# Kernel optimization log

Measured on AMD Instinct MI355X. Metric: run time of the kernel, lower is better.

Reference implementation:

```python
import jax, jax.numpy as jnp
import numpy as np


def setup_inputs() -> dict:
    key = jax.random.key(0)
    k1, k2, k3, k4 = jax.random.split(key, 4)
    H = W = 1024
    B = 16
    image = jax.random.normal(k1, (1, H, W), dtype=jnp.float32)
    x = jax.random.normal(k2, (B, 1, H, W), dtype=jnp.float32)
    # Conv2d(1, 9, 3) parameters, torch layout: weight (out=9, in=1, 3, 3), bias (9,)
    fan_in = 1 * 3 * 3
    bound = 1.0 / np.sqrt(fan_in)
    W_KL = jax.random.uniform(k3, (9, 1, 3, 3), jnp.float32, -bound, bound)
    b_KL = jax.random.uniform(k4, (9,), jnp.float32, -bound, bound)
    return {"image": image, "x": x, "W_KL": W_KL, "b_KL": b_KL}


def reference(image, x, W_KL, b_KL):
    # K = Conv2d(image): (1,H,W) -> (9,H,W), 'same' padding
    K = jax.lax.conv_general_dilated(
        image[None], W_KL, window_strides=(1, 1), padding='SAME',
        dimension_numbers=('NCHW', 'OIHW', 'NCHW'))[0] + b_KL[:, None, None]
    H, W = image.shape[1], image.shape[2]
    # permute (9,H,W) -> (H,W,9) -> unflatten to per-pixel 3x3 kernels (H,W,3,3)
    K = jnp.transpose(K, (1, 2, 0)).reshape(H, W, 3, 3)
    # Apply spatially-varying 3x3 kernel: y[b,c,h,w] = sum_{a,d} K[h,w,a,d] * x_pad[b,c,h+a,w+d]
    x_pad = jnp.pad(x, ((0, 0), (0, 0), (1, 1), (1, 1)))
    y = jnp.zeros_like(x)
    for a in range(3):
        for d in range(3):
            y = y + K[:, :, a, d] * x_pad[:, :, a:a + H, d:d + W]
    return y
```

## Files before the change

kernel.cpp:

```cpp
#include <hip/hip_runtime.h>

#define IH 1024
#define IW 1024
#define NB 16

typedef float v4f __attribute__((ext_vector_type(4)));

__device__ __forceinline__ void glds16(const float* g, float* l) {
    __builtin_amdgcn_global_load_lds(
        (const __attribute__((address_space(1))) void*)g,
        (__attribute__((address_space(3))) void*)l, 16, 0, 0);
}

struct RawWin { v4f mv[3]; float fl[3]; float fr[3]; };

__device__ __forceinline__ void issue_win(const float* __restrict__ plane,
                                          int h, int w0, RawWin& rw) {
#pragma unroll
    for (int a = 0; a < 3; ++a) {
        const int hh = h + a - 1;
        const int hc = (hh < 0) ? 0 : (hh >= IH ? IH - 1 : hh);
        const float* rowp = plane + (size_t)hc * IW;
        rw.fl[a] = rowp[w0 > 0 ? w0 - 1 : 0];
        rw.mv[a] = *(const v4f*)(rowp + w0);
        rw.fr[a] = rowp[w0 + 4 < IW ? w0 + 4 : IW - 1];
    }
}

__device__ __forceinline__ void fin_win_img(const RawWin& rw, int h, int w0,
                                            float win[3][6]) {
#pragma unroll
    for (int a = 0; a < 3; ++a) {
        const int hh = h + a - 1;
        const bool rowok = (hh >= 0) & (hh < IH);
        win[a][0] = (rowok && w0 > 0)      ? rw.fl[a]   : 0.f;
        win[a][1] = rowok ? rw.mv[a].x : 0.f;
        win[a][2] = rowok ? rw.mv[a].y : 0.f;
        win[a][3] = rowok ? rw.mv[a].z : 0.f;
        win[a][4] = rowok ? rw.mv[a].w : 0.f;
        win[a][5] = (rowok && w0 + 4 < IW) ? rw.fr[a]   : 0.f;
    }
}

__global__ __launch_bounds__(256, 4) void fused_dbuf(
    const float* __restrict__ image,
    const float* __restrict__ x,
    const float* __restrict__ Wk,
    const float* __restrict__ bk,
    float* __restrict__ out)
{
    __shared__ float lds[2][6][256];

    const int tx = threadIdx.x;
    const int wv = threadIdx.y;

    const int hwid  = blockIdx.x;
    const int xcd   = hwid & 7;
    const int chunk = hwid >> 3;
    const int bx    = chunk & 3;
    const int g     = xcd * 32 + (chunk >> 2);
    const int c0    = bx * 256;
    const int h0    = g * 4;
    const int h     = h0 + wv;
    const int lc    = tx * 4;
    const int w0    = c0 + lc;

    const size_t plane = (size_t)IH * IW;

    int zv; asm("v_mov_b32 %0, 0" : "=v"(zv));

    auto stage = [&](int b, int buf) {
        const float* xb = x + (size_t)b * plane;
        int gr = h0 - 1 + wv; gr = gr < 0 ? 0 : gr;
        glds16(xb + (size_t)gr * IW + c0 + tx * 4, &lds[buf][wv][0]);
        if (wv < 2) {
            int g2 = h0 + 3 + wv; g2 = g2 > IH - 1 ? IH - 1 : g2;
            glds16(xb + (size_t)g2 * IW + c0 + tx * 4, &lds[buf][wv + 4][0]);
        }
    };
    auto halo = [&](int b, float* HL, float* HR) {
        const float* xb = x + (size_t)b * plane;
        const int cl = (c0 > 0) ? c0 - 1 : 0;
        const int cr = (c0 + 256 < IW) ? c0 + 256 : IW - 1;
#pragma unroll
        for (int a = 0; a < 3; ++a) {
            int gr = h + a - 1; gr = gr < 0 ? 0 : (gr > IH - 1 ? IH - 1 : gr);
            const float* rp = xb + (size_t)gr * IW;
            HL[a] = rp[cl + zv];
            HR[a] = rp[cr + zv];
        }
    };

    RawWin rimg;
    issue_win(image, h, w0, rimg);
    stage(0, 0);
    float hl[2][3], hr[2][3];
    halo(0, hl[0], hr[0]);

    float wkk[81];
#pragma unroll
    for (int i = 0; i < 81; ++i) wkk[i] = Wk[i];
    float bb[9];
#pragma unroll
    for (int c = 0; c < 9; ++c) bb[c] = bk[c];

    float p[3][6];
    fin_win_img(rimg, h, w0, p);
    float Kv[4][9];
#pragma unroll
    for (int j = 0; j < 4; ++j)
#pragma unroll
        for (int c = 0; c < 9; ++c) {
            float acc = bb[c];
#pragma unroll
            for (int a = 0; a < 3; ++a)
#pragma unroll
                for (int d = 0; d < 3; ++d)
                    acc = fmaf(wkk[c * 9 + a * 3 + d], p[a][j + d], acc);
            Kv[j][c] = acc;
        }
    {
        const bool top = (h == 0);
        const bool bot = (h == IH - 1);
#pragma unroll
        for (int j = 0; j < 4; ++j)
#pragma unroll
            for (int d = 0; d < 3; ++d) {
                Kv[j][d]     = top ? 0.f : Kv[j][d];
                Kv[j][6 + d] = bot ? 0.f : Kv[j][6 + d];
            }
    }

    asm volatile("s_waitcnt vmcnt(6)" ::: "memory");
    __builtin_amdgcn_sched_barrier(0);
    __builtin_amdgcn_s_barrier();
    __builtin_amdgcn_sched_barrier(0);

    v4f yv[2];
    float* obp = out + (size_t)h * IW + w0;

#pragma unroll
    for (int b = 0; b < NB; ++b) {
        if (b > 0)
            __builtin_nontemporal_store(yv[(b - 1) & 1],
                                        (v4f*)(obp + (size_t)(b - 1) * plane));
        if (b + 1 < NB) {
            stage(b + 1, (b + 1) & 1);
            halo(b + 1, hl[(b + 1) & 1], hr[(b + 1) & 1]);
        }
        {
            const int ll = (tx > 0)  ? lc - 4 : 0;
            const int lr = (tx < 63) ? lc + 4 : 252;
            const float* lb = &lds[b & 1][0][0];
            float win[3][6];
#pragma unroll
            for (int a = 0; a < 3; ++a) {
                const float* rowp = lb + (wv + a) * 256;
                const v4f lv = *(const v4f*)(rowp + ll);
                const v4f mv = *(const v4f*)(rowp + lc);
                const v4f rv = *(const v4f*)(rowp + lr);
                const float le = (tx == 0)  ? hl[b & 1][a] : lv.w;
                const float re = (tx == 63) ? hr[b & 1][a] : rv.x;
                win[a][0] = (w0 > 0)      ? le : 0.f;
                win[a][1] = mv.x; win[a][2] = mv.y;
                win[a][3] = mv.z; win[a][4] = mv.w;
                win[a][5] = (w0 + 4 < IW) ? re : 0.f;
            }
            v4f yy;
#pragma unroll
            for (int j = 0; j < 4; ++j) {
                float acc = 0.f;
#pragma unroll
                for (int a = 0; a < 3; ++a)
#pragma unroll
                    for (int d = 0; d < 3; ++d)
                        acc = fmaf(Kv[j][a * 3 + d], win[a][j + d], acc);
                yy[j] = acc;
            }
            yv[b & 1] = yy;
        }
        if (b + 1 < NB) {
            asm volatile("s_waitcnt vmcnt(6)" ::: "memory");
            __builtin_amdgcn_sched_barrier(0);
            __builtin_amdgcn_s_barrier();
            __builtin_amdgcn_sched_barrier(0);
        }
    }
    __builtin_nontemporal_store(yv[(NB - 1) & 1],
                                (v4f*)(obp + (size_t)(NB - 1) * plane));
}

extern "C" void kernel_launch(void* const* d_in, const int* in_sizes, int n_in,
                              void* d_out, int out_size, void* d_ws, size_t ws_size,
                              hipStream_t stream) {
    const float* image = (const float*)d_in[0];
    const float* x     = (const float*)d_in[1];
    const float* Wk    = (const float*)d_in[2];
    const float* bk    = (const float*)d_in[3];
    float* out = (float*)d_out;

    dim3 block(64, 4);
    dim3 grid(1024);
    fused_dbuf<<<grid, block, 0, stream>>>(image, x, Wk, bk, out);
}
```

Before: 123.9 us.

## Give each wave private LDS rows and triple-buffer to drop workgroup barriers

Each wave now stages its own three input rows into a private LDS region instead of the block sharing six rows. Because no wave reads another wave's rows, the per-batch workgroup barriers can go, and synchronisation relies only on per-wave vmcnt waits. Prefetch distance grows from one batch to two with a three-slot buffer. The cost is about 1.5x more global-to-LDS traffic for the overlapping rows, more LDS per block, and hand-tuned vmcnt counts that are fragile if the compiler reorders memory ops.

```diff
diff --git a/kernel.cpp b/kernel.cpp
--- a/kernel.cpp
+++ b/kernel.cpp
@@ -5,6 +5,8 @@
 #define NB 16
 
 typedef float v4f __attribute__((ext_vector_type(4)));
+
+#define VMWAIT(n) asm volatile("s_waitcnt vmcnt(" #n ")" ::: "memory")
 
 __device__ __forceinline__ void glds16(const float* g, float* l) {
     __builtin_amdgcn_global_load_lds(
@@ -42,14 +44,14 @@
     }
 }
 
-__global__ __launch_bounds__(256, 4) void fused_dbuf(
+__global__ __launch_bounds__(256, 4) void fused_nobar(
     const float* __restrict__ image,
     const float* __restrict__ x,
     const float* __restrict__ Wk,
     const float* __restrict__ bk,
     float* __restrict__ out)
 {
-    __shared__ float lds[2][6][256];
+    __shared__ float lds[4][3][3][256];
 
     const int tx = threadIdx.x;
     const int wv = threadIdx.y;
@@ -60,8 +62,7 @@
     const int bx    = chunk & 3;
     const int g     = xcd * 32 + (chunk >> 2);
     const int c0    = bx * 256;
-    const int h0    = g * 4;
-    const int h     = h0 + wv;
+    const int h     = g * 4 + wv;
     const int lc    = tx * 4;
     const int w0    = c0 + lc;
 
@@ -71,11 +72,10 @@
 
     auto stage = [&](int b, int buf) {
         const float* xb = x + (size_t)b * plane;
-        int gr = h0 - 1 + wv; gr = gr < 0 ? 0 : gr;
-        glds16(xb + (size_t)gr * IW + c0 + tx * 4, &lds[buf][wv][0]);
-        if (wv < 2) {
-            int g2 = h0 + 3 + wv; g2 = g2 > IH - 1 ? IH - 1 : g2;
-            glds16(xb + (size_t)g2 * IW + c0 + tx * 4, &lds[buf][wv + 4][0]);
+#pragma unroll
+        for (int a = 0; a < 3; ++a) {
+            int gr = h + a - 1; gr = gr < 0 ? 0 : (gr > IH - 1 ? IH - 1 : gr);
+            glds16(xb + (size_t)gr * IW + c0 + tx * 4, &lds[wv][buf][a][0]);
         }
     };
     auto halo = [&](int b, float* HL, float* HR) {
@@ -93,9 +93,11 @@
 
     RawWin rimg;
     issue_win(image, h, w0, rimg);
-    stage(0, 0);
-    float hl[2][3], hr[2][3];
-    halo(0, hl[0], hr[0]);
+    __builtin_amdgcn_sched_barrier(0);
+    float hl[3][3], hr[3][3];
+    stage(0, 0); halo(0, hl[0], hr[0]);
+    stage(1, 1); halo(1, hl[1], hr[1]);
+    __builtin_amdgcn_sched_barrier(0);
 
     float wkk[81];
 #pragma unroll
@@ -131,62 +133,56 @@
             }
     }
 
-    asm volatile("s_waitcnt vmcnt(6)" ::: "memory");
-    __builtin_amdgcn_sched_barrier(0);
-    __builtin_amdgcn_s_barrier();
-    __builtin_amdgcn_sched_barrier(0);
-
-    v4f yv[2];
+    v4f yprev;
     float* obp = out + (size_t)h * IW + w0;
+    const int ll = (tx > 0)  ? lc - 4 : 0;
+    const int lr = (tx < 63) ? lc + 4 : 252;
 
 #pragma unroll
     for (int b = 0; b < NB; ++b) {
         if (b > 0)
-            __builtin_nontemporal_store(yv[(b - 1) & 1],
+            __builtin_nontemporal_store(yprev,
                                         (v4f*)(obp + (size_t)(b - 1) * plane));
-        if (b + 1 < NB) {
-            stage(b + 1, (b + 1) & 1);
-            halo(b + 1, hl[(b + 1) & 1], hr[(b + 1) & 1]);
-        }
-        {
-            const int ll = (tx > 0)  ? lc - 4 : 0;
-            const int lr = (tx < 63) ? lc + 4 : 252;
-            const float* lb = &lds[b & 1][0][0];
-            float win[3][6];
-#pragma unroll
-            for (int a = 0; a < 3; ++a) {
-                const float* rowp = lb + (wv + a) * 256;
-                const v4f lv = *(const v4f*)(rowp + ll);
-                const v4f mv = *(const v4f*)(rowp + lc);
-                const v4f rv = *(const v4f*)(rowp + lr);
-                const float le = (tx == 0)  ? hl[b & 1][a] : lv.w;
-                const float re = (tx == 63) ? hr[b & 1][a] : rv.x;
-                win[a][0] = (w0 > 0)      ? le : 0.f;
-                win[a][1] = mv.x; win[a][2] = mv.y;
-                win[a][3] = mv.z; win[a][4] = mv.w;
-                win[a][5] = (w0 + 4 < IW) ? re : 0.f;
-            }
-            v4f yy;
-#pragma unroll
-            for (int j = 0; j < 4; ++j) {
-                float acc = 0.f;
-#pragma unroll
-                for (int a = 0; a < 3; ++a)
-#pragma unroll
-                    for (int d = 0; d < 3; ++d)
-                        acc = fmaf(Kv[j][a * 3 + d], win[a][j + d], acc);
-                yy[j] = acc;
-            }
-            yv[b & 1] = yy;
-        }
-        if (b + 1 < NB) {
-            asm volatile("s_waitcnt vmcnt(6)" ::: "memory");
-            __builtin_amdgcn_sched_barrier(0);
-            __builtin_amdgcn_s_barrier();
-            __builtin_amdgcn_sched_barrier(0);
-        }
-    }
-    __builtin_nontemporal_store(yv[(NB - 1) & 1],
+        if (b + 2 < NB) {
+            stage(b + 2, (b + 2) % 3);
+            halo(b + 2, hl[(b + 2) % 3], hr[(b + 2) % 3]);
+        }
+        if      (b == 0)  VMWAIT(18);
+        else if (b == 1)  VMWAIT(19);
+        else if (b == 14) VMWAIT(11);
+        else if (b == 15) VMWAIT(2);
+        else              VMWAIT(20);
+        __builtin_amdgcn_sched_barrier(0);
+
+        const float* lb = &lds[wv][b % 3][0][0];
+        float win[3][6];
+#pragma unroll
+        for (int a = 0; a < 3; ++a) {
+            const float* rowp = lb + a * 256;
+            const v4f lv = *(const v4f*)(rowp + ll);
+            const v4f mv = *(const v4f*)(rowp + lc);
+            const v4f rv = *(const v4f*)(rowp + lr);
+            const float le = (tx == 0)  ? hl[b % 3][a] : lv.w;
+            const float re = (tx == 63) ? hr[b % 3][a] : rv.x;
+            win[a][0] = (w0 > 0)      ? le : 0.f;
+            win[a][1] = mv.x; win[a][2] = mv.y;
+            win[a][3] = mv.z; win[a][4] = mv.w;
+            win[a][5] = (w0 + 4 < IW) ? re : 0.f;
+        }
+        v4f yy;
+#pragma unroll
+        for (int j = 0; j < 4; ++j) {
+            float acc = 0.f;
+#pragma unroll
+            for (int a = 0; a < 3; ++a)
+#pragma unroll
+                for (int d = 0; d < 3; ++d)
+                    acc = fmaf(Kv[j][a * 3 + d], win[a][j + d], acc);
+            yy[j] = acc;
+        }
+        yprev = yy;
+    }
+    __builtin_nontemporal_store(yprev,
                                 (v4f*)(obp + (size_t)(NB - 1) * plane));
 }
 
@@ -201,5 +197,5 @@
 
     dim3 block(64, 4);
     dim3 grid(1024);
-    fused_dbuf<<<grid, block, 0, stream>>>(image, x, Wk, bk, out);
-}
+    fused_nobar<<<grid, block, 0, stream>>>(image, x, Wk, bk, out);
+}
```

Measured after the change: 135.1 us. 1.09x slower.

## Split batch across two blocks per tile and raise occupancy target to 8

Applied to the files above, without the earlier changes.

Each spatial tile's 16-image batch loop is now split across two blocks of 8 images each, and the grid doubles to 2048. Launch bounds are raised to 8 waves-per-EU-level occupancy. The aim is more concurrent blocks for hiding memory latency. In exchange, the per-pixel kernel coefficients (the 81-weight conv on the image) are recomputed twice as often, and register pressure is constrained by the tighter launch bound.

```diff
diff --git a/kernel.cpp b/kernel.cpp
--- a/kernel.cpp
+++ b/kernel.cpp
@@ -3,8 +3,11 @@
 #define IH 1024
 #define IW 1024
 #define NB 16
+#define NB2 8
 
 typedef float v4f __attribute__((ext_vector_type(4)));
+
+#define VMWAIT(n) asm volatile("s_waitcnt vmcnt(" #n ")" ::: "memory")
 
 __device__ __forceinline__ void glds16(const float* g, float* l) {
     __builtin_amdgcn_global_load_lds(
@@ -42,7 +45,7 @@
     }
 }
 
-__global__ __launch_bounds__(256, 4) void fused_dbuf(
+__global__ __launch_bounds__(256, 8) void fused_occ8(
     const float* __restrict__ image,
     const float* __restrict__ x,
     const float* __restrict__ Wk,
@@ -57,20 +60,22 @@
     const int hwid  = blockIdx.x;
     const int xcd   = hwid & 7;
     const int chunk = hwid >> 3;
-    const int bx    = chunk & 3;
-    const int g     = xcd * 32 + (chunk >> 2);
+    const int bz    = chunk & 1;
+    const int bx    = (chunk >> 1) & 3;
+    const int g     = xcd * 32 + (chunk >> 3);
     const int c0    = bx * 256;
     const int h0    = g * 4;
     const int h     = h0 + wv;
     const int lc    = tx * 4;
     const int w0    = c0 + lc;
+    const int b0    = bz * NB2;
 
     const size_t plane = (size_t)IH * IW;
 
     int zv; asm("v_mov_b32 %0, 0" : "=v"(zv));
 
-    auto stage = [&](int b, int buf) {
-        const float* xb = x + (size_t)b * plane;
+    auto stage = [&](int gb, int buf) {
+        const float* xb = x + (size_t)gb * plane;
         int gr = h0 - 1 + wv; gr = gr < 0 ? 0 : gr;
         glds16(xb + (size_t)gr * IW + c0 + tx * 4, &lds[buf][wv][0]);
         if (wv < 2) {
@@ -78,8 +83,8 @@
             glds16(xb + (size_t)g2 * IW + c0 + tx * 4, &lds[buf][wv + 4][0]);
         }
     };
-    auto halo = [&](int b, float* HL, float* HR) {
-        const float* xb = x + (size_t)b * plane;
+    auto halo = [&](int gb, float* HL, float* HR) {
+        const float* xb = x + (size_t)gb * plane;
         const int cl = (c0 > 0) ? c0 - 1 : 0;
         const int cr = (c0 + 256 < IW) ? c0 + 256 : IW - 1;
 #pragma unroll
@@ -93,9 +98,9 @@
 
     RawWin rimg;
     issue_win(image, h, w0, rimg);
-    stage(0, 0);
+    stage(b0, 0);
     float hl[2][3], hr[2][3];
-    halo(0, hl[0], hr[0]);
+    halo(b0, hl[0], hr[0]);
 
     float wkk[81];
 #pragma unroll
@@ -131,26 +136,27 @@
             }
     }
 
-    asm volatile("s_waitcnt vmcnt(6)" ::: "memory");
+    VMWAIT(6);
     __builtin_amdgcn_sched_barrier(0);
     __builtin_amdgcn_s_barrier();
     __builtin_amdgcn_sched_barrier(0);
 
-    v4f yv[2];
+    v4f yprev;
     float* obp = out + (size_t)h * IW + w0;
-
-#pragma unroll
-    for (int b = 0; b < NB; ++b) {
+    const int ll = (tx > 0)  ? lc - 4 : 0;
+    const int lr = (tx < 63) ? lc + 4 : 252;
+
+#pragma unroll
+    for (int b = 0; b < NB2; ++b) {
+        const int gb = b0 + b;
         if (b > 0)
-            __builtin_nontemporal_store(yv[(b - 1) & 1],
-                                        (v4f*)(obp + (size_t)(b - 1) * plane));
-        if (b + 1 < NB) {
-            stage(b + 1, (b + 1) & 1);
-            halo(b + 1, hl[(b + 1) & 1], hr[(b + 1) & 1]);
+            __builtin_nontemporal_store(yprev,
+                                        (v4f*)(obp + (size_t)(gb - 1) * plane));
+        if (b + 1 < NB2) {
+            stage(gb + 1, (b + 1) & 1);
+            halo(gb + 1, hl[(b + 1) & 1], hr[(b + 1) & 1]);
         }
         {
-            const int ll = (tx > 0)  ? lc - 4 : 0;
-            const int lr = (tx < 63) ? lc + 4 : 252;
             const float* lb = &lds[b & 1][0][0];
             float win[3][6];
 #pragma unroll
@@ -177,17 +183,17 @@
                         acc = fmaf(Kv[j][a * 3 + d], win[a][j + d], acc);
                 yy[j] = acc;
             }
-            yv[b & 1] = yy;
-        }
-        if (b + 1 < NB) {
-            asm volatile("s_waitcnt vmcnt(6)" ::: "memory");
+            yprev = yy;
+        }
+        if (b + 1 < NB2) {
+            VMWAIT(6);
             __builtin_amdgcn_sched_barrier(0);
             __builtin_amdgcn_s_barrier();
             __builtin_amdgcn_sched_barrier(0);
         }
     }
-    __builtin_nontemporal_store(yv[(NB - 1) & 1],
-                                (v4f*)(obp + (size_t)(NB - 1) * plane));
+    __builtin_nontemporal_store(yprev,
+                                (v4f*)(obp + (size_t)(b0 + NB2 - 1) * plane));
 }
 
 extern "C" void kernel_launch(void* const* d_in, const int* in_sizes, int n_in,
@@ -200,6 +206,6 @@
     float* out = (float*)d_out;
 
     dim3 block(64, 4);
-    dim3 grid(1024);
-    fused_dbuf<<<grid, block, 0, stream>>>(image, x, Wk, bk, out);
-}
+    dim3 grid(2048);
+    fused_occ8<<<grid, block, 0, stream>>>(image, x, Wk, bk, out);
+}
```

Measured after the change: 295.7 us. +138.7%, slower.
